# Performance work log

Measured on AMD Instinct MI355X. Metric: run time of the kernel, lower is better.

## Reference

```python
import jax, jax.numpy as jnp
import numpy as np

HIDDEN = 1024
NUM_HEADS = 16
HEAD_DIM = HIDDEN // NUM_HEADS
WINDOW = 64
B, S = 2, 4096


def setup_inputs() -> dict:
    key = jax.random.key(0)
    ks = jax.random.split(key, 8)
    d = {
        'query': jax.random.normal(ks[0], (B, S, HIDDEN), jnp.float32),
        'key':   jax.random.normal(ks[1], (B, S, HIDDEN), jnp.float32),
        'value': jax.random.normal(ks[2], (B, S, HIDDEN), jnp.float32),
        'Wq': jax.random.normal(ks[3], (HIDDEN, HIDDEN), jnp.float32) * 0.02,
        'bq': jnp.zeros((HIDDEN,), jnp.float32),
        'Wk': jax.random.normal(ks[4], (HIDDEN, HIDDEN), jnp.float32) * 0.02,
        'bk': jnp.zeros((HIDDEN,), jnp.float32),
        'Wv': jax.random.normal(ks[5], (HIDDEN, HIDDEN), jnp.float32) * 0.02,
        'bv': jnp.zeros((HIDDEN,), jnp.float32),
        'Wo': jax.random.normal(ks[6], (HIDDEN, HIDDEN), jnp.float32) * 0.02,
        'bo': jnp.zeros((HIDDEN,), jnp.float32),
    }
    return d


def reference(query, key, value, Wq, bq, Wk, bk, Wv, bv, Wo, bo):
    b, s, _ = query.shape
    h, d, w = NUM_HEADS, HEAD_DIM, WINDOW
    nw = s // w
    scale = d ** -0.5
    # projections (torch Linear: x @ W.T + b)
    q = (query @ Wq.T + bq).reshape(b, s, h, d).transpose(0, 2, 1, 3)  # [b,h,s,d]
    k = (key   @ Wk.T + bk).reshape(b, s, h, d).transpose(0, 2, 1, 3)
    v = (value @ Wv.T + bv).reshape(b, s, h, d).transpose(0, 2, 1, 3)
    # split into non-overlapping windows: [b,h,nw,w,d]
    qw = q.reshape(b, h, nw, w, d)
    kw = k.reshape(b, h, nw, w, d)
    vw = v.reshape(b, h, nw, w, d)
    scores = jnp.einsum('bhnqd,bhnkd->bhnqk', qw, kw) * scale  # [b,h,nw,w,w]
    weights = jax.nn.softmax(scores, axis=-1)
    attended = jnp.einsum('bhnqk,bhnkd->bhnqd', weights, vw)   # [b,h,nw,w,d]
    attended = attended.reshape(b, h, s, d).transpose(0, 2, 1, 3).reshape(b, s, h * d)
    output = attended @ Wo.T + bo
    # block-diagonal attention map, averaged over heads -> [b,s,s]
    mean_w = weights.mean(axis=1)  # [b,nw,w,w]
    full = jnp.zeros((b, nw, w, nw, w), weights.dtype)
    idx = jnp.arange(nw)
    full = full.at[:, idx, :, idx, :].set(mean_w.transpose(1, 0, 2, 3))
    attn = full.reshape(b, s, s)
    return output, attn
```

## Files before the change

kernel.cpp:

```cpp
#include <hip/hip_runtime.h>

typedef unsigned short u16;
typedef unsigned int u32;
typedef __attribute__((ext_vector_type(8))) short bf16x8;
typedef __attribute__((ext_vector_type(4))) float f32x4;
typedef __attribute__((ext_vector_type(4))) u16 u16x4;

typedef __attribute__((address_space(1))) unsigned int as1_u32;
typedef __attribute__((address_space(3))) unsigned int as3_u32;

#define SEQ 4096
#define HID 1024
#define NHEAD 16
#define BATCH 2

__device__ __forceinline__ u16 f2b(float f) {
  union { float f; u32 u; } v; v.f = f;
  u32 r = v.u + 0x7FFFu + ((v.u >> 16) & 1u);
  return (u16)(r >> 16);
}

__device__ __forceinline__ float b2f(u16 b) {
  union { u32 u; float f; } v; v.u = ((u32)b) << 16;
  return v.f;
}

__device__ __forceinline__ void async_cp16(const void* g, void* l) {
  __builtin_amdgcn_global_load_lds((const as1_u32*)g, (as3_u32*)l, 16, 0, 0);
}

__global__ __launch_bounds__(256) void cvt_all(
    const float* __restrict__ q, const float* __restrict__ k, const float* __restrict__ v,
    const float* __restrict__ Wq, const float* __restrict__ Wk,
    const float* __restrict__ Wv, const float* __restrict__ Wo,
    u16* __restrict__ xq, u16* __restrict__ xk, u16* __restrict__ xv,
    u16* __restrict__ wq, u16* __restrict__ wk, u16* __restrict__ wv, u16* __restrict__ wo) {
  const int total = (3 << 21) + (4 << 18);
  for (int i = blockIdx.x * blockDim.x + threadIdx.x; i < total; i += gridDim.x * blockDim.x) {
    const float* src; u16* dst; int j;
    if (i < (3 << 21)) {
      const int sel = i >> 21; j = i & ((1 << 21) - 1);
      src = sel == 0 ? q : (sel == 1 ? k : v);
      dst = sel == 0 ? xq : (sel == 1 ? xk : xv);
    } else {
      const int ii = i - (3 << 21);
      const int sel = ii >> 18; j = ii & ((1 << 18) - 1);
      src = sel == 0 ? Wq : (sel == 1 ? Wk : (sel == 2 ? Wv : Wo));
      dst = sel == 0 ? wq : (sel == 1 ? wk : (sel == 2 ? wv : wo));
    }
    float4 f = ((const float4*)src)[j];
    u16x4 o; o.x = f2b(f.x); o.y = f2b(f.y); o.z = f2b(f.z); o.w = f2b(f.w);
    ((u16x4*)dst)[j] = o;
  }
}

template <int MODE>
__device__ __forceinline__ void gemm_core(
    const u16* __restrict__ A, const u16* __restrict__ Bw,
    const float* __restrict__ bias, void* __restrict__ Cout,
    u16* As, u16* Bs, long brow, long bcol) {
  const int K = HID, N = HID;
  const int tid = threadIdx.x;
  const int lane = tid & 63;
  const int wave = tid >> 6;
  const int l15 = lane & 15;
  const int quad = lane >> 4;
  const int wr = wave >> 1;
  const int wc = wave & 1;

  const int srow = lane >> 2;
  const int scol = (lane & 3) * 8;
  const u16* Ag0 = A + (brow + wave * 16 + srow) * (long)K + scol;
  const u16* Ag1 = A + (brow + (wave + 4) * 16 + srow) * (long)K + scol;
  const u16* Bg0 = Bw + (bcol + wave * 16 + srow) * (long)K + scol;
  const u16* Bg1 = Bw + (bcol + (wave + 4) * 16 + srow) * (long)K + scol;
  u16* Al0 = As + wave * 512;
  u16* Al1 = As + (wave + 4) * 512;
  u16* Bl0 = Bs + wave * 512;
  u16* Bl1 = Bs + (wave + 4) * 512;

  f32x4 acc[4][4];
#pragma unroll
  for (int i = 0; i < 4; ++i)
#pragma unroll
    for (int j = 0; j < 4; ++j) acc[i][j] = f32x4{0.f, 0.f, 0.f, 0.f};

  const u16* Afb = As + (wr * 64 + l15) * 32 + quad * 8;
  const u16* Bfb = Bs + (wc * 64 + l15) * 32 + quad * 8;

  for (int k0 = 0; k0 < K; k0 += 32) {
    async_cp16(Ag0 + k0, Al0);
    async_cp16(Ag1 + k0, Al1);
    async_cp16(Bg0 + k0, Bl0);
    async_cp16(Bg1 + k0, Bl1);
    __syncthreads();
    bf16x8 af[4], bfv[4];
#pragma unroll
    for (int mt = 0; mt < 4; ++mt) af[mt] = *(const bf16x8*)(Afb + mt * 512);
#pragma unroll
    for (int nt = 0; nt < 4; ++nt) bfv[nt] = *(const bf16x8*)(Bfb + nt * 512);
#pragma unroll
    for (int mt = 0; mt < 4; ++mt)
#pragma unroll
      for (int nt = 0; nt < 4; ++nt) {
        if (MODE == 2)
          acc[mt][nt] = __builtin_amdgcn_mfma_f32_16x16x32_bf16(af[mt], bfv[nt], acc[mt][nt], 0, 0, 0);
        else
          acc[mt][nt] = __builtin_amdgcn_mfma_f32_16x16x32_bf16(bfv[nt], af[mt], acc[mt][nt], 0, 0, 0);
      }
    __syncthreads();
  }

  const long crow0 = brow + wr * 64;
  const long ccol0 = bcol + wc * 64;

  if (MODE == 2) {
#pragma unroll
    for (int nt = 0; nt < 4; ++nt) {
      const long col = ccol0 + nt * 16 + l15;
      const float bv = bias[col];
#pragma unroll
      for (int mt = 0; mt < 4; ++mt) {
        const long tokbase = crow0 + mt * 16 + quad * 4;
        const long b = tokbase >> 12;
        const long tok = tokbase & 4095;
        const long h = col >> 6, d = col & 63;
        u16x4 pk;
        pk.x = f2b(acc[mt][nt][0] + bv);
        pk.y = f2b(acc[mt][nt][1] + bv);
        pk.z = f2b(acc[mt][nt][2] + bv);
        pk.w = f2b(acc[mt][nt][3] + bv);
        *(u16x4*)((u16*)Cout + ((b * 16 + h) * 64 + d) * (long)SEQ + tok) = pk;
      }
    }
  } else {
#pragma unroll
    for (int nt = 0; nt < 4; ++nt) {
      const long colb = ccol0 + nt * 16 + quad * 4;
      const float4 b4 = *(const float4*)(bias + colb);
#pragma unroll
      for (int mt = 0; mt < 4; ++mt) {
        const long row = crow0 + mt * 16 + l15;
        if (MODE == 1) {
          float4 v;
          v.x = acc[mt][nt][0] + b4.x;
          v.y = acc[mt][nt][1] + b4.y;
          v.z = acc[mt][nt][2] + b4.z;
          v.w = acc[mt][nt][3] + b4.w;
          *(float4*)((float*)Cout + row * (long)N + colb) = v;
        } else {
          u16x4 pk;
          pk.x = f2b(acc[mt][nt][0] + b4.x);
          pk.y = f2b(acc[mt][nt][1] + b4.y);
          pk.z = f2b(acc[mt][nt][2] + b4.z);
          pk.w = f2b(acc[mt][nt][3] + b4.w);
          *(u16x4*)((u16*)Cout + row * (long)N + colb) = pk;
        }
      }
    }
  }
}

struct Gemm3Args {
  const u16* A[3]; const u16* W[3]; const float* bias[3]; void* C[3]; int mode[3];
};

__global__ __launch_bounds__(256, 2) void gemm_bt_fused(Gemm3Args ga) {
  __shared__ __align__(16) u16 As[128 * 32];
  __shared__ __align__(16) u16 Bs[128 * 32];
  const int z = blockIdx.z;
  const long brow = (long)blockIdx.y * 128;
  const long bcol = (long)blockIdx.x * 128;
  if (ga.mode[z] == 2)
    gemm_core<2>(ga.A[z], ga.W[z], ga.bias[z], ga.C[z], As, Bs, brow, bcol);
  else
    gemm_core<0>(ga.A[z], ga.W[z], ga.bias[z], ga.C[z], As, Bs, brow, bcol);
}

__global__ __launch_bounds__(256, 4) void attn_win(
    const u16* __restrict__ qp, const u16* __restrict__ kp,
    const u16* __restrict__ vT, u16* __restrict__ attended,
    float* __restrict__ Psum) {
  __shared__ __align__(16) u16 Plds[4][32][72];

  const int tid = threadIdx.x;
  const int lane = tid & 63;
  const int wave = tid >> 6;
  const int l15 = lane & 15;
  const int quad = lane >> 4;

  const int idx = blockIdx.x;
  const int half = idx & 1;
  const int hg = (idx >> 1) & 3;
  const int wn = idx >> 3;
  const int b = wn >> 6;
  const int n = wn & 63;
  const int h = hg * 4 + wave;

  const long qrow0 = (long)b * SEQ + (long)n * 64 + half * 32;
  const long krow0 = (long)b * SEQ + (long)n * 64;
  const long cbase = (long)h * 64;

  u16(*Pw)[72] = Plds[wave];

  f32x4 s[2][4];
#pragma unroll
  for (int i = 0; i < 2; ++i)
#pragma unroll
    for (int j = 0; j < 4; ++j) s[i][j] = f32x4{0.f, 0.f, 0.f, 0.f};
#pragma unroll
  for (int kt = 0; kt < 2; ++kt) {
    bf16x8 aq[2], bkf[4];
#pragma unroll
    for (int mt = 0; mt < 2; ++mt)
      aq[mt] = *(const bf16x8*)(qp + (qrow0 + mt * 16 + l15) * HID + cbase + kt * 32 + quad * 8);
#pragma unroll
    for (int nt = 0; nt < 4; ++nt)
      bkf[nt] = *(const bf16x8*)(kp + (krow0 + nt * 16 + l15) * HID + cbase + kt * 32 + quad * 8);
#pragma unroll
    for (int mt = 0; mt < 2; ++mt)
#pragma unroll
      for (int nt = 0; nt < 4; ++nt)
        s[mt][nt] = __builtin_amdgcn_mfma_f32_16x16x32_bf16(bkf[nt], aq[mt], s[mt][nt], 0, 0, 0);
  }

#pragma unroll
  for (int mt = 0; mt < 2; ++mt) {
    float m = -1e30f;
#pragma unroll
    for (int nt = 0; nt < 4; ++nt)
#pragma unroll
      for (int r = 0; r < 4; ++r) { s[mt][nt][r] *= 0.125f; m = fmaxf(m, s[mt][nt][r]); }
    m = fmaxf(m, __shfl_xor(m, 16));
    m = fmaxf(m, __shfl_xor(m, 32));
    float sum = 0.f;
#pragma unroll
    for (int nt = 0; nt < 4; ++nt)
#pragma unroll
      for (int r = 0; r < 4; ++r) { float e = __expf(s[mt][nt][r] - m); s[mt][nt][r] = e; sum += e; }
    sum += __shfl_xor(sum, 16);
    sum += __shfl_xor(sum, 32);
    const float inv = 1.f / sum;
#pragma unroll
    for (int nt = 0; nt < 4; ++nt)
#pragma unroll
      for (int r = 0; r < 4; ++r) s[mt][nt][r] *= inv;
  }

#pragma unroll
  for (int mt = 0; mt < 2; ++mt)
#pragma unroll
    for (int nt = 0; nt < 4; ++nt) {
      u16x4 pk;
      pk.x = f2b(s[mt][nt][0]);
      pk.y = f2b(s[mt][nt][1]);
      pk.z = f2b(s[mt][nt][2]);
      pk.w = f2b(s[mt][nt][3]);
      *(u16x4*)(&Pw[mt * 16 + l15][nt * 16 + quad * 4]) = pk;
    }

  f32x4 o[2][4];
#pragma unroll
  for (int i = 0; i < 2; ++i)
#pragma unroll
    for (int j = 0; j < 4; ++j) o[i][j] = f32x4{0.f, 0.f, 0.f, 0.f};
  const long vbase = ((long)(b * 16 + h) * 64) * SEQ;
#pragma unroll
  for (int kt = 0; kt < 2; ++kt) {
    bf16x8 ap[2], bvf[4];
#pragma unroll
    for (int mt = 0; mt < 2; ++mt)
      ap[mt] = *(const bf16x8*)(&Pw[mt * 16 + l15][kt * 32 + quad * 8]);
#pragma unroll
    for (int nt = 0; nt < 4; ++nt)
      bvf[nt] = *(const bf16x8*)(vT + vbase + (long)(nt * 16 + l15) * SEQ + n * 64 + kt * 32 + quad * 8);
#pragma unroll
    for (int mt = 0; mt < 2; ++mt)
#pragma unroll
      for (int nt = 0; nt < 4; ++nt)
        o[mt][nt] = __builtin_amdgcn_mfma_f32_16x16x32_bf16(bvf[nt], ap[mt], o[mt][nt], 0, 0, 0);
  }

#pragma unroll
  for (int mt = 0; mt < 2; ++mt)
#pragma unroll
    for (int nt = 0; nt < 4; ++nt) {
      const long row = qrow0 + mt * 16 + l15;
      const long col = cbase + nt * 16 + quad * 4;
      u16x4 pk;
      pk.x = f2b(o[mt][nt][0]);
      pk.y = f2b(o[mt][nt][1]);
      pk.z = f2b(o[mt][nt][2]);
      pk.w = f2b(o[mt][nt][3]);
      *(u16x4*)(attended + row * HID + col) = pk;
    }

  __syncthreads();
  float* pbase = Psum + (long)idx * 2048;
  for (int i = tid; i < 32 * 64; i += 256) {
    const int r = i >> 6, c = i & 63;
    float sacc = 0.f;
#pragma unroll
    for (int w = 0; w < 4; ++w) sacc += b2f(Plds[w][r][c]);
    pbase[i] = sacc;
  }
}

__global__ __launch_bounds__(256, 2) void gemm_o_expand(
    const u16* __restrict__ A, const u16* __restrict__ Bw,
    const float* __restrict__ bias, float* __restrict__ Cout,
    const float* __restrict__ Psum, float* __restrict__ attn) {
  __shared__ __align__(16) u16 As[128 * 32];
  __shared__ __align__(16) u16 Bs[128 * 32];

  const int tid = threadIdx.x;

  if (blockIdx.x >= 512) {
    const long e = blockIdx.x - 512;
    const long f0 = e * 4096;
#pragma unroll
    for (int it = 0; it < 16; ++it) {
      const long f = f0 + it * 256 + tid;
      const int b = (int)(f >> 22);
      const int rem = (int)(f & ((1 << 22) - 1));
      const int row = rem >> 10;
      const int c4 = rem & 1023;
      const int n = row >> 6;
      float4 val = {0.f, 0.f, 0.f, 0.f};
      const int d4 = c4 - n * 16;
      if ((unsigned)d4 < 16u) {
        const int r = row & 63;
        const int half = r >> 5, rr = r & 31;
        const long base = ((long)((b * 64 + n) * 8 + half)) * 2048 + rr * 64 + d4 * 4;
        float4 p0 = *(const float4*)(Psum + base);
        float4 p1 = *(const float4*)(Psum + base + 4096);
        float4 p2 = *(const float4*)(Psum + base + 8192);
        float4 p3 = *(const float4*)(Psum + base + 12288);
        val.x = (p0.x + p1.x + p2.x + p3.x) * (1.f / 16.f);
        val.y = (p0.y + p1.y + p2.y + p3.y) * (1.f / 16.f);
        val.z = (p0.z + p1.z + p2.z + p3.z) * (1.f / 16.f);
        val.w = (p0.w + p1.w + p2.w + p3.w) * (1.f / 16.f);
      }
      ((float4*)attn)[f] = val;
    }
    return;
  }

  const long brow = (long)(blockIdx.x >> 3) * 128;
  const long bcol = (long)(blockIdx.x & 7) * 128;
  gemm_core<1>(A, Bw, bias, Cout, As, Bs, brow, bcol);
}

extern "C" void kernel_launch(void* const* d_in, const int* in_sizes, int n_in,
                              void* d_out, int out_size, void* d_ws, size_t ws_size,
                              hipStream_t stream) {
  (void)in_sizes; (void)n_in; (void)out_size; (void)ws_size;
  const float* query = (const float*)d_in[0];
  const float* key   = (const float*)d_in[1];
  const float* value = (const float*)d_in[2];
  const float* Wq = (const float*)d_in[3];
  const float* bq = (const float*)d_in[4];
  const float* Wk = (const float*)d_in[5];
  const float* bk = (const float*)d_in[6];
  const float* Wv = (const float*)d_in[7];
  const float* bv = (const float*)d_in[8];
  const float* Wo = (const float*)d_in[9];
  const float* bo = (const float*)d_in[10];

  float* out  = (float*)d_out;
  float* attn = out + (size_t)BATCH * SEQ * HID;

  char* ws = (char*)d_ws;
  const size_t MB = (size_t)1 << 20;
  u16* xq = (u16*)(ws + 0 * MB);
  u16* xk = (u16*)(ws + 16 * MB);
  u16* xv = (u16*)(ws + 32 * MB);
  u16* wq = (u16*)(ws + 48 * MB);
  u16* wk = (u16*)(ws + 50 * MB);
  u16* wv = (u16*)(ws + 52 * MB);
  u16* wo = (u16*)(ws + 54 * MB);
  u16* qp = (u16*)(ws + 56 * MB);
  u16* kp = (u16*)(ws + 72 * MB);
  u16* vT = (u16*)(ws + 88 * MB);
  float* Psum = (float*)(ws + 104 * MB);
  u16* att = xq;

  cvt_all<<<3584, 256, 0, stream>>>(query, key, value, Wq, Wk, Wv, Wo,
                                    xq, xk, xv, wq, wk, wv, wo);

  Gemm3Args ga;
  ga.A[0] = xq; ga.W[0] = wq; ga.bias[0] = bq; ga.C[0] = qp; ga.mode[0] = 0;
  ga.A[1] = xk; ga.W[1] = wk; ga.bias[1] = bk; ga.C[1] = kp; ga.mode[1] = 0;
  ga.A[2] = xv; ga.W[2] = wv; ga.bias[2] = bv; ga.C[2] = vT; ga.mode[2] = 2;
  dim3 g3(HID / 128, (BATCH * SEQ) / 128, 3);
  gemm_bt_fused<<<g3, 256, 0, stream>>>(ga);

  attn_win<<<BATCH * 64 * 4 * 2, 256, 0, stream>>>(qp, kp, vT, att, Psum);

  gemm_o_expand<<<512 + 2048, 256, 0, stream>>>(att, wo, bo, out, Psum, attn);
}
```

Measured before the change: 391.0 us.

## Rewrite GEMM core with 4-stage async LDS pipeline, 256x128 tiles, swizzle

The GEMM core now uses 512-thread blocks computing 256x128 tiles, with a 4-deep ring of LDS buffers filled by async global-to-LDS copies. Explicit vmcnt waits let loads for three future k-tiles overlap the MFMA work on the current one. An XOR swizzle on the LDS column slot is meant to cut bank conflicts, and each wave now holds an 8x2 accumulator grid. The cost is 96KB of LDS per block and higher register pressure, which may limit occupancy. The expand blocks in the output kernel are resized to fit the new block shape.

New measurement: 414.4 us. 6.0% more time.

```diff
diff --git a/kernel.cpp b/kernel.cpp
--- a/kernel.cpp
+++ b/kernel.cpp
@@ -54,107 +54,129 @@
   }
 }
 
+
+template <int VM, int MODE>
+__device__ __forceinline__ void ktile(
+    const u16* buf, int offA, int offB, f32x4 (&acc)[8][2]) {
+  if constexpr (VM == 9)      asm volatile("s_waitcnt vmcnt(9)" ::: "memory");
+  else if constexpr (VM == 6) asm volatile("s_waitcnt vmcnt(6)" ::: "memory");
+  else if constexpr (VM == 3) asm volatile("s_waitcnt vmcnt(3)" ::: "memory");
+  else                        asm volatile("s_waitcnt vmcnt(0)" ::: "memory");
+  __builtin_amdgcn_s_barrier();
+  __builtin_amdgcn_sched_barrier(0);
+  bf16x8 af[8], bfv[2];
+#pragma unroll
+  for (int m = 0; m < 8; ++m) af[m] = *(const bf16x8*)(buf + offA + m * 512);
+#pragma unroll
+  for (int n = 0; n < 2; ++n) bfv[n] = *(const bf16x8*)(buf + offB + n * 512);
+#pragma unroll
+  for (int m = 0; m < 8; ++m)
+#pragma unroll
+    for (int n = 0; n < 2; ++n) {
+      if (MODE == 2)
+        acc[m][n] = __builtin_amdgcn_mfma_f32_16x16x32_bf16(af[m], bfv[n], acc[m][n], 0, 0, 0);
+      else
+        acc[m][n] = __builtin_amdgcn_mfma_f32_16x16x32_bf16(bfv[n], af[m], acc[m][n], 0, 0, 0);
+    }
+  asm volatile("s_waitcnt lgkmcnt(0)" ::: "memory");
+  __builtin_amdgcn_sched_barrier(0);
+  __builtin_amdgcn_s_barrier();
+}
+
 template <int MODE>
 __device__ __forceinline__ void gemm_core(
     const u16* __restrict__ A, const u16* __restrict__ Bw,
     const float* __restrict__ bias, void* __restrict__ Cout,
-    u16* As, u16* Bs, long brow, long bcol) {
-  const int K = HID, N = HID;
+    u16* lds, long brow, long bcol) {
+  const int K = HID;
   const int tid = threadIdx.x;
   const int lane = tid & 63;
   const int wave = tid >> 6;
   const int l15 = lane & 15;
   const int quad = lane >> 4;
-  const int wr = wave >> 1;
-  const int wc = wave & 1;
-
-  const int srow = lane >> 2;
-  const int scol = (lane & 3) * 8;
-  const u16* Ag0 = A + (brow + wave * 16 + srow) * (long)K + scol;
-  const u16* Ag1 = A + (brow + (wave + 4) * 16 + srow) * (long)K + scol;
-  const u16* Bg0 = Bw + (bcol + wave * 16 + srow) * (long)K + scol;
-  const u16* Bg1 = Bw + (bcol + (wave + 4) * 16 + srow) * (long)K + scol;
-  u16* Al0 = As + wave * 512;
-  u16* Al1 = As + (wave + 4) * 512;
-  u16* Bl0 = Bs + wave * 512;
-  u16* Bl1 = Bs + (wave + 4) * 512;
-
-  f32x4 acc[4][4];
-#pragma unroll
-  for (int i = 0; i < 4; ++i)
-#pragma unroll
-    for (int j = 0; j < 4; ++j) acc[i][j] = f32x4{0.f, 0.f, 0.f, 0.f};
-
-  const u16* Afb = As + (wr * 64 + l15) * 32 + quad * 8;
-  const u16* Bfb = Bs + (wc * 64 + l15) * 32 + quad * 8;
-
-  for (int k0 = 0; k0 < K; k0 += 32) {
-    async_cp16(Ag0 + k0, Al0);
-    async_cp16(Ag1 + k0, Al1);
-    async_cp16(Bg0 + k0, Bl0);
-    async_cp16(Bg1 + k0, Bl1);
-    __syncthreads();
-    bf16x8 af[4], bfv[4];
-#pragma unroll
-    for (int mt = 0; mt < 4; ++mt) af[mt] = *(const bf16x8*)(Afb + mt * 512);
-#pragma unroll
-    for (int nt = 0; nt < 4; ++nt) bfv[nt] = *(const bf16x8*)(Bfb + nt * 512);
-#pragma unroll
-    for (int mt = 0; mt < 4; ++mt)
-#pragma unroll
-      for (int nt = 0; nt < 4; ++nt) {
-        if (MODE == 2)
-          acc[mt][nt] = __builtin_amdgcn_mfma_f32_16x16x32_bf16(af[mt], bfv[nt], acc[mt][nt], 0, 0, 0);
-        else
-          acc[mt][nt] = __builtin_amdgcn_mfma_f32_16x16x32_bf16(bfv[nt], af[mt], acc[mt][nt], 0, 0, 0);
-      }
-    __syncthreads();
-  }
-
-  const long crow0 = brow + wr * 64;
-  const long ccol0 = bcol + wc * 64;
+  const int wr = wave >> 2;
+  const int wc = wave & 3;
+
+  const int rowq = tid >> 2;
+  const int slotl = (tid & 3) ^ (rowq & 3);
+  const u16* srcA0 = A + (brow + rowq) * (long)K + slotl * 8;
+  const u16* srcA1 = A + (brow + 128 + rowq) * (long)K + slotl * 8;
+  const u16* srcB  = Bw + (bcol + rowq) * (long)K + slotl * 8;
+
+  auto issue = [&](int tt) {
+    u16* dst = lds + (tt & 3) * 12288;
+    const long ko = (long)tt * 32;
+    async_cp16(srcA0 + ko, dst + wave * 512);
+    async_cp16(srcA1 + ko, dst + 4096 + wave * 512);
+    async_cp16(srcB  + ko, dst + 8192 + wave * 512);
+  };
+
+  const int swz = (quad ^ (l15 & 3)) * 8;
+  const int offA = (wr * 128 + l15) * 32 + swz;
+  const int offB = 8192 + (wc * 32 + l15) * 32 + swz;
+
+  f32x4 acc[8][2];
+#pragma unroll
+  for (int m = 0; m < 8; ++m)
+#pragma unroll
+    for (int n = 0; n < 2; ++n) acc[m][n] = f32x4{0.f, 0.f, 0.f, 0.f};
+
+  issue(0); issue(1); issue(2);
+
+  const int NT = K / 32;
+#pragma unroll 1
+  for (int t = 0; t < NT - 3; ++t) {
+    issue(t + 3);
+    ktile<9, MODE>(lds + (t & 3) * 12288, offA, offB, acc);
+  }
+  ktile<6, MODE>(lds + ((NT - 3) & 3) * 12288, offA, offB, acc);
+  ktile<3, MODE>(lds + ((NT - 2) & 3) * 12288, offA, offB, acc);
+  ktile<0, MODE>(lds + ((NT - 1) & 3) * 12288, offA, offB, acc);
+
+  const long crow0 = brow + wr * 128;
+  const long ccol0 = bcol + wc * 32;
 
   if (MODE == 2) {
 #pragma unroll
-    for (int nt = 0; nt < 4; ++nt) {
-      const long col = ccol0 + nt * 16 + l15;
+    for (int n = 0; n < 2; ++n) {
+      const long col = ccol0 + n * 16 + l15;
       const float bv = bias[col];
-#pragma unroll
-      for (int mt = 0; mt < 4; ++mt) {
-        const long tokbase = crow0 + mt * 16 + quad * 4;
+      const long h = col >> 6, d = col & 63;
+#pragma unroll
+      for (int m = 0; m < 8; ++m) {
+        const long tokbase = crow0 + m * 16 + quad * 4;
         const long b = tokbase >> 12;
         const long tok = tokbase & 4095;
-        const long h = col >> 6, d = col & 63;
         u16x4 pk;
-        pk.x = f2b(acc[mt][nt][0] + bv);
-        pk.y = f2b(acc[mt][nt][1] + bv);
-        pk.z = f2b(acc[mt][nt][2] + bv);
-        pk.w = f2b(acc[mt][nt][3] + bv);
+        pk.x = f2b(acc[m][n][0] + bv);
+        pk.y = f2b(acc[m][n][1] + bv);
+        pk.z = f2b(acc[m][n][2] + bv);
+        pk.w = f2b(acc[m][n][3] + bv);
         *(u16x4*)((u16*)Cout + ((b * 16 + h) * 64 + d) * (long)SEQ + tok) = pk;
       }
     }
   } else {
 #pragma unroll
-    for (int nt = 0; nt < 4; ++nt) {
-      const long colb = ccol0 + nt * 16 + quad * 4;
+    for (int n = 0; n < 2; ++n) {
+      const long colb = ccol0 + n * 16 + quad * 4;
       const float4 b4 = *(const float4*)(bias + colb);
 #pragma unroll
-      for (int mt = 0; mt < 4; ++mt) {
-        const long row = crow0 + mt * 16 + l15;
+      for (int m = 0; m < 8; ++m) {
+        const long row = crow0 + m * 16 + l15;
         if (MODE == 1) {
           float4 v;
-          v.x = acc[mt][nt][0] + b4.x;
-          v.y = acc[mt][nt][1] + b4.y;
-          v.z = acc[mt][nt][2] + b4.z;
-          v.w = acc[mt][nt][3] + b4.w;
-          *(float4*)((float*)Cout + row * (long)N + colb) = v;
+          v.x = acc[m][n][0] + b4.x;
+          v.y = acc[m][n][1] + b4.y;
+          v.z = acc[m][n][2] + b4.z;
+          v.w = acc[m][n][3] + b4.w;
+          *(float4*)((float*)Cout + row * (long)HID + colb) = v;
         } else {
           u16x4 pk;
-          pk.x = f2b(acc[mt][nt][0] + b4.x);
-          pk.y = f2b(acc[mt][nt][1] + b4.y);
-          pk.z = f2b(acc[mt][nt][2] + b4.z);
-          pk.w = f2b(acc[mt][nt][3] + b4.w);
-          *(u16x4*)((u16*)Cout + row * (long)N + colb) = pk;
+          pk.x = f2b(acc[m][n][0] + b4.x);
+          pk.y = f2b(acc[m][n][1] + b4.y);
+          pk.z = f2b(acc[m][n][2] + b4.z);
+          pk.w = f2b(acc[m][n][3] + b4.w);
+          *(u16x4*)((u16*)Cout + row * (long)HID + colb) = pk;
         }
       }
     }
@@ -165,16 +187,15 @@
   const u16* A[3]; const u16* W[3]; const float* bias[3]; void* C[3]; int mode[3];
 };
 
-__global__ __launch_bounds__(256, 2) void gemm_bt_fused(Gemm3Args ga) {
-  __shared__ __align__(16) u16 As[128 * 32];
-  __shared__ __align__(16) u16 Bs[128 * 32];
+__global__ __launch_bounds__(512, 2) void gemm_bt_fused(Gemm3Args ga) {
+  __shared__ __align__(16) u16 lds[4 * 12288];
   const int z = blockIdx.z;
-  const long brow = (long)blockIdx.y * 128;
+  const long brow = (long)blockIdx.y * 256;
   const long bcol = (long)blockIdx.x * 128;
   if (ga.mode[z] == 2)
-    gemm_core<2>(ga.A[z], ga.W[z], ga.bias[z], ga.C[z], As, Bs, brow, bcol);
+    gemm_core<2>(ga.A[z], ga.W[z], ga.bias[z], ga.C[z], lds, brow, bcol);
   else
-    gemm_core<0>(ga.A[z], ga.W[z], ga.bias[z], ga.C[z], As, Bs, brow, bcol);
+    gemm_core<0>(ga.A[z], ga.W[z], ga.bias[z], ga.C[z], lds, brow, bcol);
 }
 
 __global__ __launch_bounds__(256, 4) void attn_win(
@@ -306,21 +327,20 @@
   }
 }
 
-__global__ __launch_bounds__(256, 2) void gemm_o_expand(
+__global__ __launch_bounds__(512, 2) void gemm_o_expand(
     const u16* __restrict__ A, const u16* __restrict__ Bw,
     const float* __restrict__ bias, float* __restrict__ Cout,
     const float* __restrict__ Psum, float* __restrict__ attn) {
-  __shared__ __align__(16) u16 As[128 * 32];
-  __shared__ __align__(16) u16 Bs[128 * 32];
+  __shared__ __align__(16) u16 lds[4 * 12288];
 
   const int tid = threadIdx.x;
 
-  if (blockIdx.x >= 512) {
-    const long e = blockIdx.x - 512;
+  if (blockIdx.x >= 256) {
+    const long e = blockIdx.x - 256;
     const long f0 = e * 4096;
 #pragma unroll
-    for (int it = 0; it < 16; ++it) {
-      const long f = f0 + it * 256 + tid;
+    for (int it = 0; it < 8; ++it) {
+      const long f = f0 + it * 512 + tid;
       const int b = (int)(f >> 22);
       const int rem = (int)(f & ((1 << 22) - 1));
       const int row = rem >> 10;
@@ -346,9 +366,9 @@
     return;
   }
 
-  const long brow = (long)(blockIdx.x >> 3) * 128;
+  const long brow = (long)(blockIdx.x >> 3) * 256;
   const long bcol = (long)(blockIdx.x & 7) * 128;
-  gemm_core<1>(A, Bw, bias, Cout, As, Bs, brow, bcol);
+  gemm_core<1>(A, Bw, bias, Cout, lds, brow, bcol);
 }
 
 extern "C" void kernel_launch(void* const* d_in, const int* in_sizes, int n_in,
@@ -392,10 +412,10 @@
   ga.A[0] = xq; ga.W[0] = wq; ga.bias[0] = bq; ga.C[0] = qp; ga.mode[0] = 0;
   ga.A[1] = xk; ga.W[1] = wk; ga.bias[1] = bk; ga.C[1] = kp; ga.mode[1] = 0;
   ga.A[2] = xv; ga.W[2] = wv; ga.bias[2] = bv; ga.C[2] = vT; ga.mode[2] = 2;
-  dim3 g3(HID / 128, (BATCH * SEQ) / 128, 3);
-  gemm_bt_fused<<<g3, 256, 0, stream>>>(ga);
+  dim3 g3(HID / 128, (BATCH * SEQ) / 256, 3);
+  gemm_bt_fused<<<g3, 512, 0, stream>>>(ga);
 
   attn_win<<<BATCH * 64 * 4 * 2, 256, 0, stream>>>(qp, kp, vT, att, Psum);
 
-  gemm_o_expand<<<512 + 2048, 256, 0, stream>>>(att, wo, bo, out, Psum, attn);
-}
+  gemm_o_expand<<<256 + 2048, 512, 0, stream>>>(att, wo, bo, out, Psum, attn);
+}
```

## Triple-buffer GEMM K-loop with async LDS prefetch and single barrier

Applied to the files above, without the earlier changes.

Replaces the single-buffered GEMM main loop, which issued async global-to-LDS copies and then waited on two barriers per K-step, with a three-stage LDS ring. Two tiles are prefetched ahead and vmcnt waits gate each stage, so global loads overlap the MFMA work and each step needs only one barrier. LDS per block grows from 16 KB to 48 KB, which may limit occupancy, and correctness depends on the vmcnt counts matching the issued copies.

New measurement: 395.9 us. About the same (+1.3%).

```diff
diff --git a/kernel.cpp b/kernel.cpp
--- a/kernel.cpp
+++ b/kernel.cpp
@@ -54,12 +54,32 @@
   }
 }
 
+
+template <int MODE>
+__device__ __forceinline__ void kstep(
+    const u16* buf, int offA, int offB, f32x4 (&acc)[4][4]) {
+  bf16x8 af[4], bfv[4];
+#pragma unroll
+  for (int mt = 0; mt < 4; ++mt) af[mt] = *(const bf16x8*)(buf + offA + mt * 512);
+#pragma unroll
+  for (int nt = 0; nt < 4; ++nt) bfv[nt] = *(const bf16x8*)(buf + offB + nt * 512);
+#pragma unroll
+  for (int mt = 0; mt < 4; ++mt)
+#pragma unroll
+    for (int nt = 0; nt < 4; ++nt) {
+      if (MODE == 2)
+        acc[mt][nt] = __builtin_amdgcn_mfma_f32_16x16x32_bf16(af[mt], bfv[nt], acc[mt][nt], 0, 0, 0);
+      else
+        acc[mt][nt] = __builtin_amdgcn_mfma_f32_16x16x32_bf16(bfv[nt], af[mt], acc[mt][nt], 0, 0, 0);
+    }
+}
+
 template <int MODE>
 __device__ __forceinline__ void gemm_core(
     const u16* __restrict__ A, const u16* __restrict__ Bw,
     const float* __restrict__ bias, void* __restrict__ Cout,
-    u16* As, u16* Bs, long brow, long bcol) {
-  const int K = HID, N = HID;
+    u16* lds, long brow, long bcol) {
+  const int K = HID;
   const int tid = threadIdx.x;
   const int lane = tid & 63;
   const int wave = tid >> 6;
@@ -74,10 +94,21 @@
   const u16* Ag1 = A + (brow + (wave + 4) * 16 + srow) * (long)K + scol;
   const u16* Bg0 = Bw + (bcol + wave * 16 + srow) * (long)K + scol;
   const u16* Bg1 = Bw + (bcol + (wave + 4) * 16 + srow) * (long)K + scol;
-  u16* Al0 = As + wave * 512;
-  u16* Al1 = As + (wave + 4) * 512;
-  u16* Bl0 = Bs + wave * 512;
-  u16* Bl1 = Bs + (wave + 4) * 512;
+
+  u16* buf0 = lds;
+  u16* buf1 = lds + 8192;
+  u16* buf2 = lds + 16384;
+
+  auto issue = [&](int kt, u16* buf) {
+    const long ko = (long)kt * 32;
+    async_cp16(Ag0 + ko, buf + wave * 512);
+    async_cp16(Ag1 + ko, buf + (wave + 4) * 512);
+    async_cp16(Bg0 + ko, buf + 4096 + wave * 512);
+    async_cp16(Bg1 + ko, buf + 4096 + (wave + 4) * 512);
+  };
+
+  const int offA = (wr * 64 + l15) * 32 + quad * 8;
+  const int offB = 4096 + (wc * 64 + l15) * 32 + quad * 8;
 
   f32x4 acc[4][4];
 #pragma unroll
@@ -85,31 +116,34 @@
 #pragma unroll
     for (int j = 0; j < 4; ++j) acc[i][j] = f32x4{0.f, 0.f, 0.f, 0.f};
 
-  const u16* Afb = As + (wr * 64 + l15) * 32 + quad * 8;
-  const u16* Bfb = Bs + (wc * 64 + l15) * 32 + quad * 8;
-
-  for (int k0 = 0; k0 < K; k0 += 32) {
-    async_cp16(Ag0 + k0, Al0);
-    async_cp16(Ag1 + k0, Al1);
-    async_cp16(Bg0 + k0, Bl0);
-    async_cp16(Bg1 + k0, Bl1);
-    __syncthreads();
-    bf16x8 af[4], bfv[4];
-#pragma unroll
-    for (int mt = 0; mt < 4; ++mt) af[mt] = *(const bf16x8*)(Afb + mt * 512);
-#pragma unroll
-    for (int nt = 0; nt < 4; ++nt) bfv[nt] = *(const bf16x8*)(Bfb + nt * 512);
-#pragma unroll
-    for (int mt = 0; mt < 4; ++mt)
-#pragma unroll
-      for (int nt = 0; nt < 4; ++nt) {
-        if (MODE == 2)
-          acc[mt][nt] = __builtin_amdgcn_mfma_f32_16x16x32_bf16(af[mt], bfv[nt], acc[mt][nt], 0, 0, 0);
-        else
-          acc[mt][nt] = __builtin_amdgcn_mfma_f32_16x16x32_bf16(bfv[nt], af[mt], acc[mt][nt], 0, 0, 0);
-      }
-    __syncthreads();
-  }
+  issue(0, buf0);
+  issue(1, buf1);
+
+#pragma unroll 1
+  for (int i = 0; i < 10; ++i) {
+    const int t = 3 * i;
+    asm volatile("s_waitcnt vmcnt(4)" ::: "memory");
+    __builtin_amdgcn_s_barrier();
+    issue(t + 2, buf2);
+    kstep<MODE>(buf0, offA, offB, acc);
+
+    asm volatile("s_waitcnt vmcnt(4)" ::: "memory");
+    __builtin_amdgcn_s_barrier();
+    issue(t + 3, buf0);
+    kstep<MODE>(buf1, offA, offB, acc);
+
+    asm volatile("s_waitcnt vmcnt(4)" ::: "memory");
+    __builtin_amdgcn_s_barrier();
+    issue(t + 4, buf1);
+    kstep<MODE>(buf2, offA, offB, acc);
+  }
+  asm volatile("s_waitcnt vmcnt(4)" ::: "memory");
+  __builtin_amdgcn_s_barrier();
+  kstep<MODE>(buf0, offA, offB, acc);
+
+  asm volatile("s_waitcnt vmcnt(0)" ::: "memory");
+  __builtin_amdgcn_s_barrier();
+  kstep<MODE>(buf1, offA, offB, acc);
 
   const long crow0 = brow + wr * 64;
   const long ccol0 = bcol + wc * 64;
@@ -119,12 +153,12 @@
     for (int nt = 0; nt < 4; ++nt) {
       const long col = ccol0 + nt * 16 + l15;
       const float bv = bias[col];
+      const long h = col >> 6, d = col & 63;
 #pragma unroll
       for (int mt = 0; mt < 4; ++mt) {
         const long tokbase = crow0 + mt * 16 + quad * 4;
         const long b = tokbase >> 12;
         const long tok = tokbase & 4095;
-        const long h = col >> 6, d = col & 63;
         u16x4 pk;
         pk.x = f2b(acc[mt][nt][0] + bv);
         pk.y = f2b(acc[mt][nt][1] + bv);
@@ -147,14 +181,14 @@
           v.y = acc[mt][nt][1] + b4.y;
           v.z = acc[mt][nt][2] + b4.z;
           v.w = acc[mt][nt][3] + b4.w;
-          *(float4*)((float*)Cout + row * (long)N + colb) = v;
+          *(float4*)((float*)Cout + row * (long)HID + colb) = v;
         } else {
           u16x4 pk;
           pk.x = f2b(acc[mt][nt][0] + b4.x);
           pk.y = f2b(acc[mt][nt][1] + b4.y);
           pk.z = f2b(acc[mt][nt][2] + b4.z);
           pk.w = f2b(acc[mt][nt][3] + b4.w);
-          *(u16x4*)((u16*)Cout + row * (long)N + colb) = pk;
+          *(u16x4*)((u16*)Cout + row * (long)HID + colb) = pk;
         }
       }
     }
@@ -166,15 +200,14 @@
 };
 
 __global__ __launch_bounds__(256, 2) void gemm_bt_fused(Gemm3Args ga) {
-  __shared__ __align__(16) u16 As[128 * 32];
-  __shared__ __align__(16) u16 Bs[128 * 32];
+  __shared__ __align__(16) u16 lds[3 * 8192];
   const int z = blockIdx.z;
   const long brow = (long)blockIdx.y * 128;
   const long bcol = (long)blockIdx.x * 128;
   if (ga.mode[z] == 2)
-    gemm_core<2>(ga.A[z], ga.W[z], ga.bias[z], ga.C[z], As, Bs, brow, bcol);
+    gemm_core<2>(ga.A[z], ga.W[z], ga.bias[z], ga.C[z], lds, brow, bcol);
   else
-    gemm_core<0>(ga.A[z], ga.W[z], ga.bias[z], ga.C[z], As, Bs, brow, bcol);
+    gemm_core<0>(ga.A[z], ga.W[z], ga.bias[z], ga.C[z], lds, brow, bcol);
 }
 
 __global__ __launch_bounds__(256, 4) void attn_win(
@@ -310,8 +343,7 @@
     const u16* __restrict__ A, const u16* __restrict__ Bw,
     const float* __restrict__ bias, float* __restrict__ Cout,
     const float* __restrict__ Psum, float* __restrict__ attn) {
-  __shared__ __align__(16) u16 As[128 * 32];
-  __shared__ __align__(16) u16 Bs[128 * 32];
+  __shared__ __align__(16) u16 lds[3 * 8192];
 
   const int tid = threadIdx.x;
 
@@ -348,7 +380,7 @@
 
   const long brow = (long)(blockIdx.x >> 3) * 128;
   const long bcol = (long)(blockIdx.x & 7) * 128;
-  gemm_core<1>(A, Bw, bias, Cout, As, Bs, brow, bcol);
+  gemm_core<1>(A, Bw, bias, Cout, lds, brow, bcol);
 }
 
 extern "C" void kernel_launch(void* const* d_in, const int* in_sizes, int n_in,
```

## Zero attention map inside QKV GEMM launch and write only diagonal blocks later

Applied to the files above, without the earlier changes.

The zero-fill of the large [b,s,s] attention map moves into the QKV projection GEMM launch, where one of every four blocks zeroes a slice, so the bandwidth-bound fill overlaps with compute-bound GEMM tiles. The output-projection kernel then writes only the block-diagonal windows from Psum, dropping from 2048 to 128 extra blocks. Block indices in both GEMMs are remapped so that blocks scheduled near each other share A rows, which should improve L2 reuse. It relies on the zero-fill finishing before the diagonal writes, which holds because the launches are stream-ordered.

Result: no change. 389.6 us (-0.4%).

```diff
diff --git a/kernel.cpp b/kernel.cpp
--- a/kernel.cpp
+++ b/kernel.cpp
@@ -165,12 +165,29 @@
   const u16* A[3]; const u16* W[3]; const float* bias[3]; void* C[3]; int mode[3];
 };
 
-__global__ __launch_bounds__(256, 2) void gemm_bt_fused(Gemm3Args ga) {
+__global__ __launch_bounds__(256, 2) void gemm_bt_fused(Gemm3Args ga, float4* __restrict__ attnZ) {
   __shared__ __align__(16) u16 As[128 * 32];
   __shared__ __align__(16) u16 Bs[128 * 32];
-  const int z = blockIdx.z;
-  const long brow = (long)blockIdx.y * 128;
-  const long bcol = (long)blockIdx.x * 128;
+  const int id = blockIdx.x;
+  const int sub = (id >> 3) & 3;
+  const int tid = threadIdx.x;
+
+  if (sub == 3) {
+    const int fid = ((id >> 5) << 3) | (id & 7);
+    float4* dst = attnZ + (long)fid * 16384;
+    const float4 z4 = {0.f, 0.f, 0.f, 0.f};
+#pragma unroll 4
+    for (int it = 0; it < 64; ++it) dst[it * 256 + tid] = z4;
+    return;
+  }
+
+  const int c = id & 7;
+  const int k = (id >> 5) * 3 + sub;
+  const int z = k >> 6;
+  const int kk = k & 63;
+  const long brow = (long)((c << 3) + (kk >> 3)) * 128;
+  const long bcol = (long)(kk & 7) * 128;
+
   if (ga.mode[z] == 2)
     gemm_core<2>(ga.A[z], ga.W[z], ga.bias[z], ga.C[z], As, Bs, brow, bcol);
   else
@@ -306,48 +323,47 @@
   }
 }
 
-__global__ __launch_bounds__(256, 2) void gemm_o_expand(
+__global__ __launch_bounds__(256, 2) void gemm_o_diag(
     const u16* __restrict__ A, const u16* __restrict__ Bw,
     const float* __restrict__ bias, float* __restrict__ Cout,
     const float* __restrict__ Psum, float* __restrict__ attn) {
   __shared__ __align__(16) u16 As[128 * 32];
   __shared__ __align__(16) u16 Bs[128 * 32];
-
+  const int id = blockIdx.x;
   const int tid = threadIdx.x;
 
-  if (blockIdx.x >= 512) {
-    const long e = blockIdx.x - 512;
-    const long f0 = e * 4096;
-#pragma unroll
-    for (int it = 0; it < 16; ++it) {
-      const long f = f0 + it * 256 + tid;
-      const int b = (int)(f >> 22);
-      const int rem = (int)(f & ((1 << 22) - 1));
-      const int row = rem >> 10;
-      const int c4 = rem & 1023;
+  if (id >= 512) {
+    const int did = id - 512;
+#pragma unroll
+    for (int it = 0; it < 4; ++it) {
+      const int di = did * 1024 + it * 256 + tid;
+      const int b = di >> 16;
+      const int r16 = di & 65535;
+      const int row = r16 >> 4;
+      const int d4 = r16 & 15;
       const int n = row >> 6;
-      float4 val = {0.f, 0.f, 0.f, 0.f};
-      const int d4 = c4 - n * 16;
-      if ((unsigned)d4 < 16u) {
-        const int r = row & 63;
-        const int half = r >> 5, rr = r & 31;
-        const long base = ((long)((b * 64 + n) * 8 + half)) * 2048 + rr * 64 + d4 * 4;
-        float4 p0 = *(const float4*)(Psum + base);
-        float4 p1 = *(const float4*)(Psum + base + 4096);
-        float4 p2 = *(const float4*)(Psum + base + 8192);
-        float4 p3 = *(const float4*)(Psum + base + 12288);
-        val.x = (p0.x + p1.x + p2.x + p3.x) * (1.f / 16.f);
-        val.y = (p0.y + p1.y + p2.y + p3.y) * (1.f / 16.f);
-        val.z = (p0.z + p1.z + p2.z + p3.z) * (1.f / 16.f);
-        val.w = (p0.w + p1.w + p2.w + p3.w) * (1.f / 16.f);
-      }
+      const int r = row & 63;
+      const int half = r >> 5, rr = r & 31;
+      const long base = ((long)((b * 64 + n) * 8 + half)) * 2048 + rr * 64 + d4 * 4;
+      float4 p0 = *(const float4*)(Psum + base);
+      float4 p1 = *(const float4*)(Psum + base + 4096);
+      float4 p2 = *(const float4*)(Psum + base + 8192);
+      float4 p3 = *(const float4*)(Psum + base + 12288);
+      float4 val;
+      val.x = (p0.x + p1.x + p2.x + p3.x) * (1.f / 16.f);
+      val.y = (p0.y + p1.y + p2.y + p3.y) * (1.f / 16.f);
+      val.z = (p0.z + p1.z + p2.z + p3.z) * (1.f / 16.f);
+      val.w = (p0.w + p1.w + p2.w + p3.w) * (1.f / 16.f);
+      const long f = ((long)b << 22) | ((long)row << 10) | ((long)n << 4) | d4;
       ((float4*)attn)[f] = val;
     }
     return;
   }
 
-  const long brow = (long)(blockIdx.x >> 3) * 128;
-  const long bcol = (long)(blockIdx.x & 7) * 128;
+  const int c = id & 7;
+  const int k = id >> 3;
+  const long brow = (long)((c << 3) + (k >> 3)) * 128;
+  const long bcol = (long)(k & 7) * 128;
   gemm_core<1>(A, Bw, bias, Cout, As, Bs, brow, bcol);
 }
 
@@ -392,10 +408,9 @@
   ga.A[0] = xq; ga.W[0] = wq; ga.bias[0] = bq; ga.C[0] = qp; ga.mode[0] = 0;
   ga.A[1] = xk; ga.W[1] = wk; ga.bias[1] = bk; ga.C[1] = kp; ga.mode[1] = 0;
   ga.A[2] = xv; ga.W[2] = wv; ga.bias[2] = bv; ga.C[2] = vT; ga.mode[2] = 2;
-  dim3 g3(HID / 128, (BATCH * SEQ) / 128, 3);
-  gemm_bt_fused<<<g3, 256, 0, stream>>>(ga);
+  gemm_bt_fused<<<2048, 256, 0, stream>>>(ga, (float4*)attn);
 
   attn_win<<<BATCH * 64 * 4 * 2, 256, 0, stream>>>(qp, kp, vT, att, Psum);
 
-  gemm_o_expand<<<512 + 2048, 256, 0, stream>>>(att, wo, bo, out, Psum, attn);
-}
+  gemm_o_diag<<<512 + 128, 256, 0, stream>>>(att, wo, bo, out, Psum, attn);
+}
```
